# Kernel optimization log

Hardware: AMD Instinct MI355X
Metric: run time of the kernel (lower is better)

## Reference

```python
import jax, jax.numpy as jnp
import numpy as np

EPS_ATTN = 1e-6
EPS_LN = 1e-5


def _layer_norm(x, g, b):
    m = jnp.mean(x, axis=-1, keepdims=True)
    v = jnp.mean((x - m) ** 2, axis=-1, keepdims=True)
    return (x - m) * jax.lax.rsqrt(v + EPS_LN) * g + b


def _linear_attention(q, k, v):
    # q,k,v: [N, L/S, H, D]; elu feature map (+1 keeps values positive)
    q = jax.nn.elu(q) + 1.0
    k = jax.nn.elu(k) + 1.0
    s_len = v.shape[1]
    v = v / s_len
    kv = jnp.einsum('nshd,nshv->nhdv', k, v)            # [N,H,D,D]
    z = 1.0 / (jnp.einsum('nlhd,nhd->nlh', q, k.sum(axis=1)) + EPS_ATTN)
    out = jnp.einsum('nlhd,nhdv->nlhv', q, kv) * z[..., None] * s_len
    return out


def setup_inputs() -> dict:
    key = jax.random.key(0)
    ks = jax.random.split(key, 8)
    N, L, S, H, D = 4, 4096, 4096, 8, 64
    sc = 0.05
    return {
        'x': jax.random.normal(ks[0], (N, L, H, D), jnp.float32),
        'source': jax.random.normal(ks[1], (N, S, H, D), jnp.float32),
        'wq': jax.random.normal(ks[2], (D, D), jnp.float32) * sc,
        'wk': jax.random.normal(ks[3], (D, D), jnp.float32) * sc,
        'wv': jax.random.normal(ks[4], (D, D), jnp.float32) * sc,
        'wmerge': jax.random.normal(ks[5], (D, D), jnp.float32) * sc,
        'w1': jax.random.normal(ks[6], (2 * D, 2 * D), jnp.float32) * sc,
        'w2': jax.random.normal(ks[7], (D, 2 * D), jnp.float32) * sc,
        'g1': jnp.ones((D,), jnp.float32),
        'b1': jnp.zeros((D,), jnp.float32),
        'g2': jnp.ones((D,), jnp.float32),
        'b2': jnp.zeros((D,), jnp.float32),
    }


def reference(x, source, wq, wk, wv, wmerge, w1, w2, g1, b1, g2, b2):
    # projections (torch Linear: y = x @ W.T), applied on last dim D=d_model
    q = jnp.einsum('nlhd,ed->nlhe', x, wq)
    k = jnp.einsum('nshd,ed->nshe', source, wk)
    v = jnp.einsum('nshd,ed->nshe', source, wv)
    message = _linear_attention(q, k, v)                # [N,L,H,D]
    message = jnp.einsum('nlhd,ed->nlhe', message, wmerge)
    message = _layer_norm(message, g1, b1)
    h = jnp.concatenate([x, message], axis=-1)          # [N,L,H,2D]
    h = jax.nn.relu(jnp.einsum('nlhd,ed->nlhe', h, w1))
    h = jnp.einsum('nlhd,ed->nlhe', h, w2)              # [N,L,H,D]
    h = _layer_norm(h, g2, b2)
    return x + h
```

## Files before the change

kernel.cpp:

```cpp
#include <hip/hip_runtime.h>
#include <cstdint>

#define NB 4
#define LL 4096
#define SS 4096
#define HH 8
#define DD 64
#define NHC (NB*HH)
#define KVCH 16

typedef unsigned short ushort_t;
typedef __bf16 bf16x8 __attribute__((ext_vector_type(8)));
typedef float f32x4 __attribute__((ext_vector_type(4)));
typedef unsigned short u16x8 __attribute__((ext_vector_type(8)));
typedef unsigned short u16x4 __attribute__((ext_vector_type(4)));

__device__ __forceinline__ float bf2f(unsigned short u) {
    union { unsigned int i; float f; } v; v.i = ((unsigned int)u) << 16; return v.f;
}
__device__ __forceinline__ unsigned short f2bf(float f) {
    union { __bf16 b; unsigned short u; } v; v.b = (__bf16)f; return v.u;
}
__device__ __forceinline__ bool input_is_bf16(const void* g1) {
    return ((const unsigned short*)g1)[0] == 0x3F80u;
}

template<bool BF16>
__device__ __forceinline__ float ldgf(const void* p, size_t i) {
    if constexpr (BF16) return bf2f(((const unsigned short*)p)[i]);
    else                return ((const float*)p)[i];
}
template<bool BF16>
__device__ __forceinline__ u16x8 ld8(const void* p, size_t i) {
    if constexpr (BF16) {
        return *reinterpret_cast<const u16x8*>((const unsigned short*)p + i);
    } else {
        const f32x4* f4 = reinterpret_cast<const f32x4*>((const float*)p + i);
        f32x4 a = f4[0], b = f4[1];
        u16x8 o;
        #pragma unroll
        for (int j = 0; j < 4; ++j) { o[j] = f2bf(a[j]); o[4 + j] = f2bf(b[j]); }
        return o;
    }
}
__device__ __forceinline__ bf16x8 ldsA(const ushort_t* p) {
    return *reinterpret_cast<const bf16x8*>(p);
}
#define MFMA16(a,b,c) __builtin_amdgcn_mfma_f32_16x16x32_bf16(a,b,c,0,0,0)

__device__ __forceinline__ int sw64(int r, int c)  { return (r << 6) + (c ^ ((r & 7) << 3)); }
__device__ __forceinline__ int sw128(int r, int c) { return (r << 7) + (c ^ ((r & 7) << 3)); }

template<bool BF16, int LC>
__device__ __forceinline__ void stage_w(const void* g, size_t goff, ushort_t* dst,
                                        int rows, int dstride, int tid) {
    int total8 = (rows << LC) >> 3;
    for (int i8 = tid; i8 < total8; i8 += 256) {
        int i = i8 << 3;
        int r = i >> LC, c = i & ((1 << LC) - 1);
        *reinterpret_cast<u16x8*>(dst + r * dstride + c) = ld8<BF16>(g, goff + i);
    }
}
template<bool BF16, int LC, int NT>
__device__ __forceinline__ void stage_sw(const void* g, ushort_t* dst, int rows, int tid) {
    int total8 = (rows << LC) >> 3;
    for (int i8 = tid; i8 < total8; i8 += NT) {
        int i = i8 << 3;
        int r = i >> LC, c = i & ((1 << LC) - 1);
        int off;
        if constexpr (LC == 6) off = sw64(r, c); else off = sw128(r, c);
        *reinterpret_cast<u16x8*>(dst + off) = ld8<BF16>(g, i);
    }
}

__device__ __forceinline__ void red16(float v[4]) {
    #pragma unroll
    for (int m = 1; m < 16; m <<= 1) {
        #pragma unroll
        for (int r = 0; r < 4; ++r) v[r] += __shfl_xor(v[r], m);
    }
}

template<bool BF16, bool PART>
__device__ void kv_body(const void* __restrict__ src, const void* __restrict__ wk,
                        const void* __restrict__ wv, float* __restrict__ kvg,
                        float* __restrict__ ksumg,
                        ushort_t* S, ushort_t* KT, ushort_t* VT, float* KS)
{
    const int tid = threadIdx.x;
    const int lane = tid & 63, w = tid >> 6;
    const int lg = lane >> 4, l15 = lane & 15;
    const int bid = blockIdx.x;
    const int nh = bid >> 4, ch = bid & 15;
    const int n = nh >> 3, h = nh & 7;
    const int s0 = ch * 256;
    const f32x4 z4 = {0.f, 0.f, 0.f, 0.f};

    stage_w<BF16, 6>(wk, 0, KT, 64, 136, tid);
    stage_w<BF16, 6>(wv, 0, VT, 64, 136, tid);
    for (int i8 = tid; i8 < 1024; i8 += 256) {
        int r = i8 >> 3, c8 = (i8 & 7) << 3;
        size_t gb = ((size_t)((size_t)n * SS + (s0 + r)) * HH + h) * DD + c8;
        *reinterpret_cast<u16x8*>(S + r * 72 + c8) = ld8<BF16>(src, gb);
    }
    __syncthreads();

    bf16x8 wkf[2][4], wvf[2][4];
    #pragma unroll
    for (int ks = 0; ks < 2; ++ks)
        #pragma unroll
        for (int nt = 0; nt < 4; ++nt) {
            wkf[ks][nt] = ldsA(KT + (nt * 16 + l15) * 136 + ks * 32 + lg * 8);
            wvf[ks][nt] = ldsA(VT + (nt * 16 + l15) * 136 + ks * 32 + lg * 8);
        }
    __syncthreads();

    f32x4 kvacc[4];
    #pragma unroll
    for (int nt = 0; nt < 4; ++nt) kvacc[nt] = z4;
    float ksp[4] = {0.f, 0.f, 0.f, 0.f};

    for (int st = 0; st < 2; ++st) {
        #pragma unroll
        for (int mtt = 0; mtt < 2; ++mtt) {
            const int rowA = w * 32 + mtt * 16;
            bf16x8 af[2];
            #pragma unroll
            for (int ks = 0; ks < 2; ++ks)
                af[ks] = ldsA(S + (rowA + l15) * 72 + ks * 32 + lg * 8);
            f32x4 ka[4], va[4];
            #pragma unroll
            for (int nt = 0; nt < 4; ++nt) { ka[nt] = z4; va[nt] = z4; }
            __builtin_amdgcn_s_setprio(1);
            #pragma unroll
            for (int ks = 0; ks < 2; ++ks)
                #pragma unroll
                for (int nt = 0; nt < 4; ++nt) {
                    ka[nt] = MFMA16(af[ks], wkf[ks][nt], ka[nt]);
                    va[nt] = MFMA16(af[ks], wvf[ks][nt], va[nt]);
                }
            __builtin_amdgcn_s_setprio(0);
            #pragma unroll
            for (int nt = 0; nt < 4; ++nt) {
                u16x4 kp, vp;
                #pragma unroll
                for (int r = 0; r < 4; ++r) {
                    float kvl = ka[nt][r];
                    kvl = kvl > 0.f ? kvl + 1.f : __expf(kvl);
                    ksp[nt] += kvl;
                    kp[r] = f2bf(kvl);
                    vp[r] = f2bf(va[nt][r]);
                }
                const int dcol = nt * 16 + l15;
                *reinterpret_cast<u16x4*>(KT + dcol * 136 + rowA + lg * 4) = kp;
                *reinterpret_cast<u16x4*>(VT + dcol * 136 + rowA + lg * 4) = vp;
            }
        }
        __syncthreads();

        if (st == 0) {
            for (int i8 = tid; i8 < 1024; i8 += 256) {
                int r = i8 >> 3, c8 = (i8 & 7) << 3;
                size_t gb = ((size_t)((size_t)n * SS + (s0 + 128 + r)) * HH + h) * DD + c8;
                *reinterpret_cast<u16x8*>(S + r * 72 + c8) = ld8<BF16>(src, gb);
            }
        }
        __builtin_amdgcn_s_setprio(1);
        #pragma unroll
        for (int ks = 0; ks < 4; ++ks) {
            bf16x8 akv = ldsA(KT + (w * 16 + l15) * 136 + ks * 32 + lg * 8);
            #pragma unroll
            for (int nt = 0; nt < 4; ++nt) {
                bf16x8 bkv = ldsA(VT + (nt * 16 + l15) * 136 + ks * 32 + lg * 8);
                kvacc[nt] = MFMA16(akv, bkv, kvacc[nt]);
            }
        }
        __builtin_amdgcn_s_setprio(0);
        __syncthreads();
    }

    if constexpr (PART) {
        float* kvo = kvg + (size_t)bid * 4096;
        #pragma unroll
        for (int nt = 0; nt < 4; ++nt)
            #pragma unroll
            for (int r = 0; r < 4; ++r)
                kvo[(w * 16 + lg * 4 + r) * DD + nt * 16 + l15] = kvacc[nt][r];
    } else {
        float* kvo = kvg + (size_t)nh * 4096;
        #pragma unroll
        for (int nt = 0; nt < 4; ++nt)
            #pragma unroll
            for (int r = 0; r < 4; ++r)
                atomicAdd(&kvo[(w * 16 + lg * 4 + r) * DD + nt * 16 + l15], kvacc[nt][r]);
    }
    #pragma unroll
    for (int m = 16; m < 64; m <<= 1)
        #pragma unroll
        for (int nt = 0; nt < 4; ++nt) ksp[nt] += __shfl_xor(ksp[nt], m);
    if (lane < 16) {
        #pragma unroll
        for (int nt = 0; nt < 4; ++nt) KS[w * 64 + nt * 16 + lane] = ksp[nt];
    }
    __syncthreads();
    if (tid < 64) {
        float s = KS[tid] + KS[64 + tid] + KS[128 + tid] + KS[192 + tid];
        if constexpr (PART) ksumg[(size_t)bid * 64 + tid] = s;
        else                atomicAdd(&ksumg[nh * 64 + tid], s);
    }
}

template<bool PART>
__global__ __launch_bounds__(256, 2) void kv_kernel(
    const void* __restrict__ src, const void* __restrict__ wk, const void* __restrict__ wv,
    const void* __restrict__ g1, float* __restrict__ kvg, float* __restrict__ ksumg)
{
    __shared__ ushort_t S[128 * 72];
    __shared__ ushort_t KT[64 * 136];
    __shared__ ushort_t VT[64 * 136];
    __shared__ float    KS[4 * 64];
    if (input_is_bf16(g1)) kv_body<true , PART>(src, wk, wv, kvg, ksumg, S, KT, VT, KS);
    else                   kv_body<false, PART>(src, wk, wv, kvg, ksumg, S, KT, VT, KS);
}

template<bool BF16, int NCH>
__device__ void reduce_body(const float* __restrict__ kvp, const float* __restrict__ ksp,
                            const void* __restrict__ wm,
                            ushort_t* __restrict__ kvmT, float* __restrict__ ksumf,
                            ushort_t* KVS, ushort_t* WMS)
{
    const int tid = threadIdx.x;
    const int lane = tid & 63, w = tid >> 6;
    const int lg = lane >> 4, l15 = lane & 15;
    const int nh = blockIdx.x;
    const f32x4 z4 = {0.f, 0.f, 0.f, 0.f};

    stage_w<BF16, 6>(wm, 0, WMS, 64, 72, tid);
    for (int i4 = tid; i4 < 1024; i4 += 256) {
        const float* base = kvp + (size_t)nh * NCH * 4096 + i4 * 4;
        f32x4 s = z4;
        #pragma unroll
        for (int c = 0; c < NCH; ++c)
            s += *reinterpret_cast<const f32x4*>(base + c * 4096);
        int d = i4 >> 4, e4 = (i4 & 15) * 4;
        u16x4 pk;
        #pragma unroll
        for (int j = 0; j < 4; ++j) pk[j] = f2bf(s[j]);
        *reinterpret_cast<u16x4*>(KVS + d * 72 + e4) = pk;
    }
    if (tid < 64) {
        float s = 0.f;
        #pragma unroll
        for (int c = 0; c < NCH; ++c) s += ksp[((size_t)nh * NCH + c) * 64 + tid];
        ksumf[nh * 64 + tid] = s;
    }
    __syncthreads();

    bf16x8 akv[2];
    #pragma unroll
    for (int ks = 0; ks < 2; ++ks)
        akv[ks] = ldsA(KVS + (w * 16 + l15) * 72 + ks * 32 + lg * 8);
    f32x4 km[4];
    #pragma unroll
    for (int nt = 0; nt < 4; ++nt) km[nt] = z4;
    #pragma unroll
    for (int ks = 0; ks < 2; ++ks)
        #pragma unroll
        for (int nt = 0; nt < 4; ++nt) {
            bf16x8 bwm = ldsA(WMS + (nt * 16 + l15) * 72 + ks * 32 + lg * 8);
            km[nt] = MFMA16(akv[ks], bwm, km[nt]);
        }
    #pragma unroll
    for (int nt = 0; nt < 4; ++nt) {
        u16x4 pk;
        #pragma unroll
        for (int r = 0; r < 4; ++r) pk[r] = f2bf(km[nt][r]);
        *reinterpret_cast<u16x4*>(kvmT + (size_t)nh * 4096 + (nt * 16 + l15) * 64
                                  + w * 16 + lg * 4) = pk;
    }
}

template<int NCH>
__global__ __launch_bounds__(256, 4) void reduce_kernel(
    const float* __restrict__ kvp, const float* __restrict__ ksp,
    const void* __restrict__ wm, const void* __restrict__ g1,
    ushort_t* __restrict__ kvmT, float* __restrict__ ksumf)
{
    __shared__ ushort_t KVS[64 * 72];
    __shared__ ushort_t WMS[64 * 72];
    if (input_is_bf16(g1)) reduce_body<true , NCH>(kvp, ksp, wm, kvmT, ksumf, KVS, WMS);
    else                   reduce_body<false, NCH>(kvp, ksp, wm, kvmT, ksumf, KVS, WMS);
}

template<bool BF16>
__device__ void main_body(const void* __restrict__ x,
                          const void* __restrict__ wq,
                          const void* __restrict__ w1, const void* __restrict__ w2,
                          const void* __restrict__ g1, const void* __restrict__ b1,
                          const void* __restrict__ g2, const void* __restrict__ b2,
                          const ushort_t* __restrict__ kvmT,
                          const float* __restrict__ ksumf,
                          void* __restrict__ outp,
                          ushort_t* W1S, ushort_t* W2S, ushort_t* WQS,
                          ushort_t* KVMS, ushort_t* B0, ushort_t* B1, ushort_t* B2)
{
    const int tid = threadIdx.x;
    const int lane = tid & 63, w = tid >> 6;
    const int lg = lane >> 4, l15 = lane & 15;
    const int bid = blockIdx.x;
    const int nh = bid >> 3, ch = bid & 7;
    const int n = nh >> 3, h = nh & 7;
    const int rowA = w * 16;
    const f32x4 z4 = {0.f, 0.f, 0.f, 0.f};

    auto ldx = [&](int p, u16x8 xv[2]) {
        #pragma unroll
        for (int pp = 0; pp < 2; ++pp) {
            int r16 = pp * 8 + (lane >> 3), c8 = (lane & 7) << 3;
            size_t gb = ((size_t)((size_t)n * LL + (ch * 512 + p * 256 + rowA + r16)) * HH + h) * DD + c8;
            xv[pp] = ld8<BF16>(x, gb);
        }
    };

    u16x8 xv[2];
    ldx(0, xv);

    stage_sw<BF16, 6, 1024>(wq, WQS, 64, tid);
    stage_sw<BF16, 7, 1024>(w2, W2S, 64, tid);
    stage_sw<BF16, 7, 1024>(w1, W1S, 128, tid);
    stage_sw<true, 6, 1024>((const void*)(kvmT + (size_t)nh * 4096), KVMS, 64, tid);
    float g1r[4], b1r[4], g2r[4], b2r[4], ksr[4];
    #pragma unroll
    for (int nt = 0; nt < 4; ++nt) {
        int c = nt * 16 + l15;
        g1r[nt] = ldgf<BF16>(g1, c); b1r[nt] = ldgf<BF16>(b1, c);
        g2r[nt] = ldgf<BF16>(g2, c); b2r[nt] = ldgf<BF16>(b2, c);
        ksr[nt] = ksumf[nh * 64 + c];
    }
    __syncthreads();

    for (int p = 0; p < 2; ++p) {
        const int l0 = ch * 512 + p * 256;

        #pragma unroll
        for (int pp = 0; pp < 2; ++pp) {
            int r16 = pp * 8 + (lane >> 3), c8 = (lane & 7) << 3;
            *reinterpret_cast<u16x8*>(B0 + sw64(rowA + r16, c8)) = xv[pp];
        }
        u16x8 xn[2];
        if (p == 0) ldx(1, xn);

        bf16x8 af[2];
        #pragma unroll
        for (int ks = 0; ks < 2; ++ks)
            af[ks] = ldsA(B0 + sw64(rowA + l15, ks * 32 + lg * 8));
        f32x4 qa[4];
        #pragma unroll
        for (int nt = 0; nt < 4; ++nt) qa[nt] = z4;
        __builtin_amdgcn_s_setprio(1);
        #pragma unroll
        for (int ks = 0; ks < 2; ++ks)
            #pragma unroll
            for (int nt = 0; nt < 4; ++nt)
                qa[nt] = MFMA16(af[ks], ldsA(WQS + sw64(nt * 16 + l15, ks * 32 + lg * 8)), qa[nt]);
        __builtin_amdgcn_s_setprio(0);
        float zp[4] = {0.f, 0.f, 0.f, 0.f};
        #pragma unroll
        for (int nt = 0; nt < 4; ++nt)
            #pragma unroll
            for (int r = 0; r < 4; ++r) {
                float v = qa[nt][r];
                v = v > 0.f ? v + 1.f : __expf(v);
                zp[r] += v * ksr[nt];
                B1[sw64(rowA + lg * 4 + r, nt * 16 + l15)] = f2bf(v);
            }
        red16(zp);
        float zr[4];
        #pragma unroll
        for (int r = 0; r < 4; ++r) zr[r] = 1.f / (zp[r] + 1e-6f);

        #pragma unroll
        for (int ks = 0; ks < 2; ++ks)
            af[ks] = ldsA(B1 + sw64(rowA + l15, ks * 32 + lg * 8));
        f32x4 ma[4];
        #pragma unroll
        for (int nt = 0; nt < 4; ++nt) ma[nt] = z4;
        __builtin_amdgcn_s_setprio(1);
        #pragma unroll
        for (int ks = 0; ks < 2; ++ks)
            #pragma unroll
            for (int nt = 0; nt < 4; ++nt)
                ma[nt] = MFMA16(af[ks], ldsA(KVMS + sw64(nt * 16 + l15, ks * 32 + lg * 8)), ma[nt]);
        __builtin_amdgcn_s_setprio(0);
        #pragma unroll
        for (int nt = 0; nt < 4; ++nt)
            #pragma unroll
            for (int r = 0; r < 4; ++r) ma[nt][r] *= zr[r];

        float s1[4] = {0.f,0.f,0.f,0.f}, s2[4] = {0.f,0.f,0.f,0.f};
        #pragma unroll
        for (int nt = 0; nt < 4; ++nt)
            #pragma unroll
            for (int r = 0; r < 4; ++r) {
                float v = ma[nt][r]; s1[r] += v; s2[r] += v * v;
            }
        red16(s1); red16(s2);
        #pragma unroll
        for (int r = 0; r < 4; ++r) {
            float mu = s1[r] * 0.015625f;
            float var = s2[r] * 0.015625f - mu * mu;
            s1[r] = mu; s2[r] = rsqrtf(var + 1e-5f);
        }
        #pragma unroll
        for (int nt = 0; nt < 4; ++nt)
            #pragma unroll
            for (int r = 0; r < 4; ++r)
                B1[sw64(rowA + lg * 4 + r, nt * 16 + l15)] =
                    f2bf((ma[nt][r] - s1[r]) * s2[r] * g1r[nt] + b1r[nt]);

        f32x4 ha[4];
        #pragma unroll
        for (int nt = 0; nt < 4; ++nt) ha[nt] = z4;
        #pragma unroll
        for (int q = 0; q < 4; ++q) {
            f32x4 ta[2];
            ta[0] = z4; ta[1] = z4;
            __builtin_amdgcn_s_setprio(1);
            #pragma unroll
            for (int ks = 0; ks < 4; ++ks) {
                const ushort_t* bp = (ks < 2) ? B0 : B1;
                bf16x8 a1 = ldsA(bp + sw64(rowA + l15, (ks & 1) * 32 + lg * 8));
                #pragma unroll
                for (int nt = 0; nt < 2; ++nt)
                    ta[nt] = MFMA16(a1, ldsA(W1S + sw128(q * 32 + nt * 16 + l15, ks * 32 + lg * 8)), ta[nt]);
            }
            __builtin_amdgcn_s_setprio(0);
            #pragma unroll
            for (int nt = 0; nt < 2; ++nt)
                #pragma unroll
                for (int r = 0; r < 4; ++r)
                    B2[(rowA + lg * 4 + r) * 40 + nt * 16 + l15] =
                        f2bf(fmaxf(ta[nt][r], 0.f));
            bf16x8 a2 = ldsA(B2 + (rowA + l15) * 40 + lg * 8);
            __builtin_amdgcn_s_setprio(1);
            #pragma unroll
            for (int nt = 0; nt < 4; ++nt)
                ha[nt] = MFMA16(a2, ldsA(W2S + sw128(nt * 16 + l15, q * 32 + lg * 8)), ha[nt]);
            __builtin_amdgcn_s_setprio(0);
        }

        float t1[4] = {0.f,0.f,0.f,0.f}, t2[4] = {0.f,0.f,0.f,0.f};
        #pragma unroll
        for (int nt = 0; nt < 4; ++nt)
            #pragma unroll
            for (int r = 0; r < 4; ++r) {
                float v = ha[nt][r]; t1[r] += v; t2[r] += v * v;
            }
        red16(t1); red16(t2);
        #pragma unroll
        for (int r = 0; r < 4; ++r) {
            float mu = t1[r] * 0.015625f;
            float var = t2[r] * 0.015625f - mu * mu;
            t1[r] = mu; t2[r] = rsqrtf(var + 1e-5f);
        }
        #pragma unroll
        for (int nt = 0; nt < 4; ++nt)
            #pragma unroll
            for (int r = 0; r < 4; ++r) {
                float xv2 = bf2f(B0[sw64(rowA + lg * 4 + r, nt * 16 + l15)]);
                float ov = xv2 + (ha[nt][r] - t1[r]) * t2[r] * g2r[nt] + b2r[nt];
                B1[sw64(rowA + lg * 4 + r, nt * 16 + l15)] = f2bf(ov);
            }

        #pragma unroll
        for (int pp = 0; pp < 2; ++pp) {
            int r16 = pp * 8 + (lane >> 3), c8 = (lane & 7) << 3;
            size_t gb = ((size_t)((size_t)n * LL + (l0 + rowA + r16)) * HH + h) * DD + c8;
            u16x8 v = *reinterpret_cast<const u16x8*>(B1 + sw64(rowA + r16, c8));
            if constexpr (BF16) {
                *reinterpret_cast<u16x8*>((unsigned short*)outp + gb) = v;
            } else {
                float* fo = (float*)outp + gb;
                f32x4 lo, hi;
                #pragma unroll
                for (int j = 0; j < 4; ++j) { lo[j] = bf2f(v[j]); hi[j] = bf2f(v[4 + j]); }
                *reinterpret_cast<f32x4*>(fo) = lo;
                *reinterpret_cast<f32x4*>(fo + 4) = hi;
            }
        }

        if (p == 0) { xv[0] = xn[0]; xv[1] = xn[1]; }
    }
}

__global__ __launch_bounds__(1024) void main_kernel(
    const void* __restrict__ x,
    const void* __restrict__ wq,
    const void* __restrict__ w1, const void* __restrict__ w2,
    const void* __restrict__ g1, const void* __restrict__ b1,
    const void* __restrict__ g2, const void* __restrict__ b2,
    const ushort_t* __restrict__ kvmT, const float* __restrict__ ksumf,
    void* __restrict__ outp)
{
    __shared__ ushort_t W1S[128 * 128];
    __shared__ ushort_t W2S[64 * 128];
    __shared__ ushort_t WQS[64 * 64];
    __shared__ ushort_t KVMS[64 * 64];
    __shared__ ushort_t B0[256 * 64];
    __shared__ ushort_t B1[256 * 64];
    __shared__ ushort_t B2[256 * 40];
    if (input_is_bf16(g1))
        main_body<true >(x, wq, w1, w2, g1, b1, g2, b2, kvmT, ksumf, outp,
                         W1S, W2S, WQS, KVMS, B0, B1, B2);
    else
        main_body<false>(x, wq, w1, w2, g1, b1, g2, b2, kvmT, ksumf, outp,
                         W1S, W2S, WQS, KVMS, B0, B1, B2);
}

extern "C" void kernel_launch(void* const* d_in, const int* in_sizes, int n_in,
                              void* d_out, int out_size, void* d_ws, size_t ws_size,
                              hipStream_t stream) {
    const void* x   = d_in[0];
    const void* src = d_in[1];
    const void* wq  = d_in[2];
    const void* wk  = d_in[3];
    const void* wv  = d_in[4];
    const void* wm  = d_in[5];
    const void* w1  = d_in[6];
    const void* w2  = d_in[7];
    const void* g1  = d_in[8];
    const void* b1  = d_in[9];
    const void* g2  = d_in[10];
    const void* b2  = d_in[11];

    const size_t kv16   = (size_t)NHC * KVCH * 4096;
    const size_t ks16   = (size_t)NHC * KVCH * 64;
    const size_t need16 = (kv16 + ks16) * sizeof(float) + (size_t)NHC * 4096 * 2
                        + (size_t)NHC * 64 * sizeof(float);

    if (ws_size >= need16) {
        float*    kvp   = (float*)d_ws;
        float*    ksp   = kvp + kv16;
        ushort_t* kvmT  = (ushort_t*)(ksp + ks16);
        float*    ksumf = (float*)(kvmT + (size_t)NHC * 4096);
        kv_kernel<true ><<<NHC * KVCH, 256, 0, stream>>>(src, wk, wv, g1, kvp, ksp);
        reduce_kernel<KVCH><<<NHC, 256, 0, stream>>>(kvp, ksp, wm, g1, kvmT, ksumf);
        main_kernel<<<NHC * 8, 1024, 0, stream>>>(x, wq, w1, w2, g1, b1, g2, b2,
                                                  kvmT, ksumf, d_out);
    } else {
        const size_t kv1 = (size_t)NHC * 4096;
        const size_t ks1 = (size_t)NHC * 64;
        float*    kvp   = (float*)d_ws;
        float*    ksp   = kvp + kv1;
        ushort_t* kvmT  = (ushort_t*)(ksp + ks1);
        float*    ksumf = (float*)(kvmT + (size_t)NHC * 4096);
        hipMemsetAsync(d_ws, 0, (kv1 + ks1) * sizeof(float), stream);
        kv_kernel<false><<<NHC * KVCH, 256, 0, stream>>>(src, wk, wv, g1, kvp, ksp);
        reduce_kernel<1><<<NHC, 256, 0, stream>>>(kvp, ksp, wm, g1, kvmT, ksumf);
        main_kernel<<<NHC * 8, 1024, 0, stream>>>(x, wq, w1, w2, g1, b1, g2, b2,
                                                  kvmT, ksumf, d_out);
    }
}
```

Baseline: 167.5 us.

## Fuse KV, reduce and main kernels into one cooperative kernel with grid syncs

Merges the three launches (KV projection/accumulation, partial reduction with merge weight, main attention+MLP) into one cooperative kernel of 256 blocks × 1024 threads, separated by grid-wide syncs. The KV phase now handles 512 source rows per block with swizzled LDS layouts and one MFMA tile per wave, and the reduction is done by half the blocks. This removes launch gaps and the intermediate kernel boundaries. In exchange it adds two grid barriers, leaves blocks idle during the reduce phase, and requires all 256 large blocks to be co-resident.

```diff
diff --git a/kernel.cpp b/kernel.cpp
--- a/kernel.cpp
+++ b/kernel.cpp
@@ -1,5 +1,8 @@
 #include <hip/hip_runtime.h>
+#include <hip/hip_cooperative_groups.h>
 #include <cstdint>
+
+namespace cg = cooperative_groups;
 
 #define NB 4
 #define LL 4096
@@ -7,7 +10,6 @@
 #define HH 8
 #define DD 64
 #define NHC (NB*HH)
-#define KVCH 16
 
 typedef unsigned short ushort_t;
 typedef __bf16 bf16x8 __attribute__((ext_vector_type(8)));
@@ -50,21 +52,12 @@
 
 __device__ __forceinline__ int sw64(int r, int c)  { return (r << 6) + (c ^ ((r & 7) << 3)); }
 __device__ __forceinline__ int sw128(int r, int c) { return (r << 7) + (c ^ ((r & 7) << 3)); }
+__device__ __forceinline__ int sw256(int r, int c) { return (r << 8) + (c ^ ((r & 7) << 3)); }
 
 template<bool BF16, int LC>
-__device__ __forceinline__ void stage_w(const void* g, size_t goff, ushort_t* dst,
-                                        int rows, int dstride, int tid) {
-    int total8 = (rows << LC) >> 3;
-    for (int i8 = tid; i8 < total8; i8 += 256) {
-        int i = i8 << 3;
-        int r = i >> LC, c = i & ((1 << LC) - 1);
-        *reinterpret_cast<u16x8*>(dst + r * dstride + c) = ld8<BF16>(g, goff + i);
-    }
-}
-template<bool BF16, int LC, int NT>
 __device__ __forceinline__ void stage_sw(const void* g, ushort_t* dst, int rows, int tid) {
     int total8 = (rows << LC) >> 3;
-    for (int i8 = tid; i8 < total8; i8 += NT) {
+    for (int i8 = tid; i8 < total8; i8 += 1024) {
         int i = i8 << 3;
         int r = i >> LC, c = i & ((1 << LC) - 1);
         int off;
@@ -81,53 +74,56 @@
     }
 }
 
-template<bool BF16, bool PART>
-__device__ void kv_body(const void* __restrict__ src, const void* __restrict__ wk,
-                        const void* __restrict__ wv, float* __restrict__ kvg,
-                        float* __restrict__ ksumg,
-                        ushort_t* S, ushort_t* KT, ushort_t* VT, float* KS)
+template<bool BF16>
+__device__ void fused_body(const void* __restrict__ x, const void* __restrict__ src,
+                           const void* __restrict__ wq, const void* __restrict__ wk,
+                           const void* __restrict__ wv, const void* __restrict__ wm,
+                           const void* __restrict__ w1, const void* __restrict__ w2,
+                           const void* __restrict__ g1, const void* __restrict__ b1,
+                           const void* __restrict__ g2, const void* __restrict__ b2,
+                           float* __restrict__ kvp, float* __restrict__ kspart,
+                           ushort_t* __restrict__ kvmT, float* __restrict__ ksumf,
+                           void* __restrict__ outp, ushort_t* LB)
 {
+    ushort_t* W1S  = LB;
+    ushort_t* W2S  = LB + 16384;
+    ushort_t* WQS  = LB + 24576;
+    ushort_t* KVMS = LB + 28672;
+    ushort_t* B0   = LB + 32768;
+    ushort_t* B1   = LB + 49152;
+    ushort_t* B2   = LB + 65536;
+    ushort_t* S = W1S;  ushort_t* KT = B0;  ushort_t* VT = B1;
+    ushort_t* WKS = WQS; ushort_t* WVS = KVMS;
+    float* KSf = (float*)B2;
+
     const int tid = threadIdx.x;
     const int lane = tid & 63, w = tid >> 6;
     const int lg = lane >> 4, l15 = lane & 15;
     const int bid = blockIdx.x;
-    const int nh = bid >> 4, ch = bid & 15;
+    const int nh = bid >> 3, ch = bid & 7;
     const int n = nh >> 3, h = nh & 7;
-    const int s0 = ch * 256;
     const f32x4 z4 = {0.f, 0.f, 0.f, 0.f};
 
-    stage_w<BF16, 6>(wk, 0, KT, 64, 136, tid);
-    stage_w<BF16, 6>(wv, 0, VT, 64, 136, tid);
-    for (int i8 = tid; i8 < 1024; i8 += 256) {
-        int r = i8 >> 3, c8 = (i8 & 7) << 3;
-        size_t gb = ((size_t)((size_t)n * SS + (s0 + r)) * HH + h) * DD + c8;
-        *reinterpret_cast<u16x8*>(S + r * 72 + c8) = ld8<BF16>(src, gb);
-    }
-    __syncthreads();
-
-    bf16x8 wkf[2][4], wvf[2][4];
-    #pragma unroll
-    for (int ks = 0; ks < 2; ++ks)
-        #pragma unroll
-        for (int nt = 0; nt < 4; ++nt) {
-            wkf[ks][nt] = ldsA(KT + (nt * 16 + l15) * 136 + ks * 32 + lg * 8);
-            wvf[ks][nt] = ldsA(VT + (nt * 16 + l15) * 136 + ks * 32 + lg * 8);
-        }
-    __syncthreads();
-
-    f32x4 kvacc[4];
-    #pragma unroll
-    for (int nt = 0; nt < 4; ++nt) kvacc[nt] = z4;
+    stage_sw<BF16, 6>(wk, WKS, 64, tid);
+    stage_sw<BF16, 6>(wv, WVS, 64, tid);
+    const int mq = w >> 2, nq = w & 3;
+    f32x4 kvacc = z4;
     float ksp[4] = {0.f, 0.f, 0.f, 0.f};
 
-    for (int st = 0; st < 2; ++st) {
-        #pragma unroll
-        for (int mtt = 0; mtt < 2; ++mtt) {
-            const int rowA = w * 32 + mtt * 16;
+    for (int p = 0; p < 2; ++p) {
+        for (int i8 = tid; i8 < 2048; i8 += 1024) {
+            int r = i8 >> 3, c8 = (i8 & 7) << 3;
+            size_t gb = ((size_t)((size_t)n * SS + (ch * 512 + p * 256 + r)) * HH + h) * DD + c8;
+            *reinterpret_cast<u16x8*>(S + sw64(r, c8)) = ld8<BF16>(src, gb);
+        }
+        __syncthreads();
+
+        {
+            const int rw = w * 16;
             bf16x8 af[2];
             #pragma unroll
             for (int ks = 0; ks < 2; ++ks)
-                af[ks] = ldsA(S + (rowA + l15) * 72 + ks * 32 + lg * 8);
+                af[ks] = ldsA(S + sw64(rw + l15, ks * 32 + lg * 8));
             f32x4 ka[4], va[4];
             #pragma unroll
             for (int nt = 0; nt < 4; ++nt) { ka[nt] = z4; va[nt] = z4; }
@@ -136,8 +132,8 @@
             for (int ks = 0; ks < 2; ++ks)
                 #pragma unroll
                 for (int nt = 0; nt < 4; ++nt) {
-                    ka[nt] = MFMA16(af[ks], wkf[ks][nt], ka[nt]);
-                    va[nt] = MFMA16(af[ks], wvf[ks][nt], va[nt]);
+                    ka[nt] = MFMA16(af[ks], ldsA(WKS + sw64(nt * 16 + l15, ks * 32 + lg * 8)), ka[nt]);
+                    va[nt] = MFMA16(af[ks], ldsA(WVS + sw64(nt * 16 + l15, ks * 32 + lg * 8)), va[nt]);
                 }
             __builtin_amdgcn_s_setprio(0);
             #pragma unroll
@@ -151,48 +147,29 @@
                     kp[r] = f2bf(kvl);
                     vp[r] = f2bf(va[nt][r]);
                 }
-                const int dcol = nt * 16 + l15;
-                *reinterpret_cast<u16x4*>(KT + dcol * 136 + rowA + lg * 4) = kp;
-                *reinterpret_cast<u16x4*>(VT + dcol * 136 + rowA + lg * 4) = vp;
+                const int dcol = nt * 16 + l15, krow = rw + lg * 4;
+                *reinterpret_cast<u16x4*>(KT + sw256(dcol, krow)) = kp;
+                *reinterpret_cast<u16x4*>(VT + sw256(dcol, krow)) = vp;
             }
         }
         __syncthreads();
 
-        if (st == 0) {
-            for (int i8 = tid; i8 < 1024; i8 += 256) {
-                int r = i8 >> 3, c8 = (i8 & 7) << 3;
-                size_t gb = ((size_t)((size_t)n * SS + (s0 + 128 + r)) * HH + h) * DD + c8;
-                *reinterpret_cast<u16x8*>(S + r * 72 + c8) = ld8<BF16>(src, gb);
-            }
-        }
         __builtin_amdgcn_s_setprio(1);
         #pragma unroll
-        for (int ks = 0; ks < 4; ++ks) {
-            bf16x8 akv = ldsA(KT + (w * 16 + l15) * 136 + ks * 32 + lg * 8);
-            #pragma unroll
-            for (int nt = 0; nt < 4; ++nt) {
-                bf16x8 bkv = ldsA(VT + (nt * 16 + l15) * 136 + ks * 32 + lg * 8);
-                kvacc[nt] = MFMA16(akv, bkv, kvacc[nt]);
-            }
+        for (int kk = 0; kk < 8; ++kk) {
+            bf16x8 ak = ldsA(KT + sw256(mq * 16 + l15, kk * 32 + lg * 8));
+            bf16x8 bv = ldsA(VT + sw256(nq * 16 + l15, kk * 32 + lg * 8));
+            kvacc = MFMA16(ak, bv, kvacc);
         }
         __builtin_amdgcn_s_setprio(0);
         __syncthreads();
     }
 
-    if constexpr (PART) {
-        float* kvo = kvg + (size_t)bid * 4096;
-        #pragma unroll
-        for (int nt = 0; nt < 4; ++nt)
-            #pragma unroll
-            for (int r = 0; r < 4; ++r)
-                kvo[(w * 16 + lg * 4 + r) * DD + nt * 16 + l15] = kvacc[nt][r];
-    } else {
-        float* kvo = kvg + (size_t)nh * 4096;
-        #pragma unroll
-        for (int nt = 0; nt < 4; ++nt)
-            #pragma unroll
-            for (int r = 0; r < 4; ++r)
-                atomicAdd(&kvo[(w * 16 + lg * 4 + r) * DD + nt * 16 + l15], kvacc[nt][r]);
+    {
+        float* kvo = kvp + (size_t)bid * 4096;
+        #pragma unroll
+        for (int r = 0; r < 4; ++r)
+            kvo[(mq * 16 + lg * 4 + r) * 64 + nq * 16 + l15] = kvacc[r];
     }
     #pragma unroll
     for (int m = 16; m < 64; m <<= 1)
@@ -200,118 +177,70 @@
         for (int nt = 0; nt < 4; ++nt) ksp[nt] += __shfl_xor(ksp[nt], m);
     if (lane < 16) {
         #pragma unroll
-        for (int nt = 0; nt < 4; ++nt) KS[w * 64 + nt * 16 + lane] = ksp[nt];
+        for (int nt = 0; nt < 4; ++nt) KSf[w * 64 + nt * 16 + lane] = ksp[nt];
     }
     __syncthreads();
     if (tid < 64) {
-        float s = KS[tid] + KS[64 + tid] + KS[128 + tid] + KS[192 + tid];
-        if constexpr (PART) ksumg[(size_t)bid * 64 + tid] = s;
-        else                atomicAdd(&ksumg[nh * 64 + tid], s);
-    }
-}
-
-template<bool PART>
-__global__ __launch_bounds__(256, 2) void kv_kernel(
-    const void* __restrict__ src, const void* __restrict__ wk, const void* __restrict__ wv,
-    const void* __restrict__ g1, float* __restrict__ kvg, float* __restrict__ ksumg)
-{
-    __shared__ ushort_t S[128 * 72];
-    __shared__ ushort_t KT[64 * 136];
-    __shared__ ushort_t VT[64 * 136];
-    __shared__ float    KS[4 * 64];
-    if (input_is_bf16(g1)) kv_body<true , PART>(src, wk, wv, kvg, ksumg, S, KT, VT, KS);
-    else                   kv_body<false, PART>(src, wk, wv, kvg, ksumg, S, KT, VT, KS);
-}
-
-template<bool BF16, int NCH>
-__device__ void reduce_body(const float* __restrict__ kvp, const float* __restrict__ ksp,
-                            const void* __restrict__ wm,
-                            ushort_t* __restrict__ kvmT, float* __restrict__ ksumf,
-                            ushort_t* KVS, ushort_t* WMS)
-{
-    const int tid = threadIdx.x;
-    const int lane = tid & 63, w = tid >> 6;
-    const int lg = lane >> 4, l15 = lane & 15;
-    const int nh = blockIdx.x;
-    const f32x4 z4 = {0.f, 0.f, 0.f, 0.f};
-
-    stage_w<BF16, 6>(wm, 0, WMS, 64, 72, tid);
-    for (int i4 = tid; i4 < 1024; i4 += 256) {
-        const float* base = kvp + (size_t)nh * NCH * 4096 + i4 * 4;
-        f32x4 s = z4;
-        #pragma unroll
-        for (int c = 0; c < NCH; ++c)
-            s += *reinterpret_cast<const f32x4*>(base + c * 4096);
-        int d = i4 >> 4, e4 = (i4 & 15) * 4;
-        u16x4 pk;
-        #pragma unroll
-        for (int j = 0; j < 4; ++j) pk[j] = f2bf(s[j]);
-        *reinterpret_cast<u16x4*>(KVS + d * 72 + e4) = pk;
-    }
-    if (tid < 64) {
         float s = 0.f;
         #pragma unroll
-        for (int c = 0; c < NCH; ++c) s += ksp[((size_t)nh * NCH + c) * 64 + tid];
-        ksumf[nh * 64 + tid] = s;
-    }
-    __syncthreads();
-
-    bf16x8 akv[2];
-    #pragma unroll
-    for (int ks = 0; ks < 2; ++ks)
-        akv[ks] = ldsA(KVS + (w * 16 + l15) * 72 + ks * 32 + lg * 8);
-    f32x4 km[4];
-    #pragma unroll
-    for (int nt = 0; nt < 4; ++nt) km[nt] = z4;
-    #pragma unroll
-    for (int ks = 0; ks < 2; ++ks)
+        for (int ww = 0; ww < 16; ++ww) s += KSf[ww * 64 + tid];
+        kspart[(size_t)bid * 64 + tid] = s;
+    }
+    __threadfence();
+    cg::this_grid().sync();
+
+    if ((bid & 7) < 4 && tid < 64) {
+        const int nh2 = bid >> 3, q4 = bid & 3;
+        const int d0 = q4 * 16;
+        f32x4 sa[2][2];
+        #pragma unroll
+        for (int ks = 0; ks < 2; ++ks) { sa[ks][0] = z4; sa[ks][1] = z4; }
+        #pragma unroll
+        for (int c = 0; c < 8; ++c) {
+            const float* base = kvp + ((size_t)nh2 * 8 + c) * 4096 + (d0 + l15) * 64;
+            #pragma unroll
+            for (int ks = 0; ks < 2; ++ks) {
+                const f32x4* p4 = reinterpret_cast<const f32x4*>(base + ks * 32 + lg * 8);
+                sa[ks][0] += p4[0];
+                sa[ks][1] += p4[1];
+            }
+        }
+        bf16x8 af[2];
+        #pragma unroll
+        for (int ks = 0; ks < 2; ++ks)
+            #pragma unroll
+            for (int j = 0; j < 8; ++j)
+                af[ks][j] = (__bf16)((j < 4) ? sa[ks][0][j] : sa[ks][1][j - 4]);
+        f32x4 km[4];
+        #pragma unroll
+        for (int nt = 0; nt < 4; ++nt) km[nt] = z4;
+        #pragma unroll
+        for (int ks = 0; ks < 2; ++ks)
+            #pragma unroll
+            for (int nt = 0; nt < 4; ++nt) {
+                u16x8 t = ld8<BF16>(wm, (size_t)(nt * 16 + l15) * 64 + ks * 32 + lg * 8);
+                bf16x8 bwm = *reinterpret_cast<bf16x8*>(&t);
+                km[nt] = MFMA16(af[ks], bwm, km[nt]);
+            }
         #pragma unroll
         for (int nt = 0; nt < 4; ++nt) {
-            bf16x8 bwm = ldsA(WMS + (nt * 16 + l15) * 72 + ks * 32 + lg * 8);
-            km[nt] = MFMA16(akv[ks], bwm, km[nt]);
-        }
-    #pragma unroll
-    for (int nt = 0; nt < 4; ++nt) {
-        u16x4 pk;
-        #pragma unroll
-        for (int r = 0; r < 4; ++r) pk[r] = f2bf(km[nt][r]);
-        *reinterpret_cast<u16x4*>(kvmT + (size_t)nh * 4096 + (nt * 16 + l15) * 64
-                                  + w * 16 + lg * 4) = pk;
-    }
-}
-
-template<int NCH>
-__global__ __launch_bounds__(256, 4) void reduce_kernel(
-    const float* __restrict__ kvp, const float* __restrict__ ksp,
-    const void* __restrict__ wm, const void* __restrict__ g1,
-    ushort_t* __restrict__ kvmT, float* __restrict__ ksumf)
-{
-    __shared__ ushort_t KVS[64 * 72];
-    __shared__ ushort_t WMS[64 * 72];
-    if (input_is_bf16(g1)) reduce_body<true , NCH>(kvp, ksp, wm, kvmT, ksumf, KVS, WMS);
-    else                   reduce_body<false, NCH>(kvp, ksp, wm, kvmT, ksumf, KVS, WMS);
-}
-
-template<bool BF16>
-__device__ void main_body(const void* __restrict__ x,
-                          const void* __restrict__ wq,
-                          const void* __restrict__ w1, const void* __restrict__ w2,
-                          const void* __restrict__ g1, const void* __restrict__ b1,
-                          const void* __restrict__ g2, const void* __restrict__ b2,
-                          const ushort_t* __restrict__ kvmT,
-                          const float* __restrict__ ksumf,
-                          void* __restrict__ outp,
-                          ushort_t* W1S, ushort_t* W2S, ushort_t* WQS,
-                          ushort_t* KVMS, ushort_t* B0, ushort_t* B1, ushort_t* B2)
-{
-    const int tid = threadIdx.x;
-    const int lane = tid & 63, w = tid >> 6;
-    const int lg = lane >> 4, l15 = lane & 15;
-    const int bid = blockIdx.x;
-    const int nh = bid >> 3, ch = bid & 7;
-    const int n = nh >> 3, h = nh & 7;
+            u16x4 pk;
+            #pragma unroll
+            for (int r = 0; r < 4; ++r) pk[r] = f2bf(km[nt][r]);
+            *reinterpret_cast<u16x4*>(kvmT + (size_t)nh2 * 4096 + (nt * 16 + l15) * 64
+                                      + d0 + lg * 4) = pk;
+        }
+        if (q4 == 0) {
+            float s = 0.f;
+            #pragma unroll
+            for (int c = 0; c < 8; ++c) s += kspart[((size_t)nh2 * 8 + c) * 64 + lane];
+            ksumf[nh2 * 64 + lane] = s;
+        }
+    }
+    __threadfence();
+    cg::this_grid().sync();
+
     const int rowA = w * 16;
-    const f32x4 z4 = {0.f, 0.f, 0.f, 0.f};
 
     auto ldx = [&](int p, u16x8 xv[2]) {
         #pragma unroll
@@ -325,10 +254,10 @@
     u16x8 xv[2];
     ldx(0, xv);
 
-    stage_sw<BF16, 6, 1024>(wq, WQS, 64, tid);
-    stage_sw<BF16, 7, 1024>(w2, W2S, 64, tid);
-    stage_sw<BF16, 7, 1024>(w1, W1S, 128, tid);
-    stage_sw<true, 6, 1024>((const void*)(kvmT + (size_t)nh * 4096), KVMS, 64, tid);
+    stage_sw<BF16, 6>(wq, WQS, 64, tid);
+    stage_sw<BF16, 7>(w2, W2S, 64, tid);
+    stage_sw<BF16, 7>(w1, W1S, 128, tid);
+    stage_sw<true, 6>((const void*)(kvmT + (size_t)nh * 4096), KVMS, 64, tid);
     float g1r[4], b1r[4], g2r[4], b2r[4], ksr[4];
     #pragma unroll
     for (int nt = 0; nt < 4; ++nt) {
@@ -493,28 +422,24 @@
     }
 }
 
-__global__ __launch_bounds__(1024) void main_kernel(
-    const void* __restrict__ x,
-    const void* __restrict__ wq,
+__global__ void __launch_bounds__(1024) fused_kernel(
+    const void* __restrict__ x, const void* __restrict__ src,
+    const void* __restrict__ wq, const void* __restrict__ wk,
+    const void* __restrict__ wv, const void* __restrict__ wm,
     const void* __restrict__ w1, const void* __restrict__ w2,
     const void* __restrict__ g1, const void* __restrict__ b1,
     const void* __restrict__ g2, const void* __restrict__ b2,
-    const ushort_t* __restrict__ kvmT, const float* __restrict__ ksumf,
+    float* __restrict__ kvp, float* __restrict__ kspart,
+    ushort_t* __restrict__ kvmT, float* __restrict__ ksumf,
     void* __restrict__ outp)
 {
-    __shared__ ushort_t W1S[128 * 128];
-    __shared__ ushort_t W2S[64 * 128];
-    __shared__ ushort_t WQS[64 * 64];
-    __shared__ ushort_t KVMS[64 * 64];
-    __shared__ ushort_t B0[256 * 64];
-    __shared__ ushort_t B1[256 * 64];
-    __shared__ ushort_t B2[256 * 40];
+    __shared__ ushort_t LB[75776];
     if (input_is_bf16(g1))
-        main_body<true >(x, wq, w1, w2, g1, b1, g2, b2, kvmT, ksumf, outp,
-                         W1S, W2S, WQS, KVMS, B0, B1, B2);
+        fused_body<true >(x, src, wq, wk, wv, wm, w1, w2, g1, b1, g2, b2,
+                          kvp, kspart, kvmT, ksumf, outp, LB);
     else
-        main_body<false>(x, wq, w1, w2, g1, b1, g2, b2, kvmT, ksumf, outp,
-                         W1S, W2S, WQS, KVMS, B0, B1, B2);
+        fused_body<false>(x, src, wq, wk, wv, wm, w1, w2, g1, b1, g2, b2,
+                          kvp, kspart, kvmT, ksumf, outp, LB);
 }
 
 extern "C" void kernel_launch(void* const* d_in, const int* in_sizes, int n_in,
@@ -533,31 +458,17 @@
     const void* g2  = d_in[10];
     const void* b2  = d_in[11];
 
-    const size_t kv16   = (size_t)NHC * KVCH * 4096;
-    const size_t ks16   = (size_t)NHC * KVCH * 64;
-    const size_t need16 = (kv16 + ks16) * sizeof(float) + (size_t)NHC * 4096 * 2
-                        + (size_t)NHC * 64 * sizeof(float);
-
-    if (ws_size >= need16) {
-        float*    kvp   = (float*)d_ws;
-        float*    ksp   = kvp + kv16;
-        ushort_t* kvmT  = (ushort_t*)(ksp + ks16);
-        float*    ksumf = (float*)(kvmT + (size_t)NHC * 4096);
-        kv_kernel<true ><<<NHC * KVCH, 256, 0, stream>>>(src, wk, wv, g1, kvp, ksp);
-        reduce_kernel<KVCH><<<NHC, 256, 0, stream>>>(kvp, ksp, wm, g1, kvmT, ksumf);
-        main_kernel<<<NHC * 8, 1024, 0, stream>>>(x, wq, w1, w2, g1, b1, g2, b2,
-                                                  kvmT, ksumf, d_out);
-    } else {
-        const size_t kv1 = (size_t)NHC * 4096;
-        const size_t ks1 = (size_t)NHC * 64;
-        float*    kvp   = (float*)d_ws;
-        float*    ksp   = kvp + kv1;
-        ushort_t* kvmT  = (ushort_t*)(ksp + ks1);
-        float*    ksumf = (float*)(kvmT + (size_t)NHC * 4096);
-        hipMemsetAsync(d_ws, 0, (kv1 + ks1) * sizeof(float), stream);
-        kv_kernel<false><<<NHC * KVCH, 256, 0, stream>>>(src, wk, wv, g1, kvp, ksp);
-        reduce_kernel<1><<<NHC, 256, 0, stream>>>(kvp, ksp, wm, g1, kvmT, ksumf);
-        main_kernel<<<NHC * 8, 1024, 0, stream>>>(x, wq, w1, w2, g1, b1, g2, b2,
-                                                  kvmT, ksumf, d_out);
-    }
-}
+    float*    kvp    = (float*)d_ws;
+    float*    kspart = kvp + (size_t)256 * 4096;
+    ushort_t* kvmT   = (ushort_t*)(kspart + (size_t)256 * 64);
+    float*    ksumf  = (float*)(kvmT + (size_t)NHC * 4096);
+    void*     outp   = d_out;
+
+    void* args[] = {
+        (void*)&x, (void*)&src, (void*)&wq, (void*)&wk, (void*)&wv, (void*)&wm,
+        (void*)&w1, (void*)&w2, (void*)&g1, (void*)&b1, (void*)&g2, (void*)&b2,
+        (void*)&kvp, (void*)&kspart, (void*)&kvmT, (void*)&ksumf, (void*)&outp
+    };
+    hipLaunchCooperativeKernel((const void*)fused_kernel, dim3(256), dim3(1024),
+                               args, 0, stream);
+}
```

Measured after the change: 397.2 us. 137% more time.
